# Performance work log

Measured on AMD Instinct MI355X. Metric: run time of the kernel, lower is better.

Reference implementation:

```python
import jax, jax.numpy as jnp
import numpy as np

B, HW, D, CL, K, V, NL, H = 16, 4096, 512, 768, 512, 512, 32, 8
EPS = 1e-5

def conv1d(x, w, b):
    # 1x1 Conv1d: x (B, Cin, L), w (Cout, Cin), b (Cout,)
    return jnp.einsum('oi,bil->bol', w, x) + b[:, None]

def inorm(x):
    # InstanceNorm1d (affine=False, biased var) over the length dim per channel
    m = jnp.mean(x, axis=-1, keepdims=True)
    v = jnp.var(x, axis=-1, keepdims=True)
    return (x - m) / jnp.sqrt(v + EPS)

def _forward(x, l, l_mask, w_vis, b_vis, w_langp, b_langp, w_q, b_q, w_k, b_k,
             w_v, b_v, w_lv, b_lv, w_W, b_W, w_langW, b_langW,
             w_mm, b_mm, w_langmm, b_langmm):
    xt = x.transpose(0, 2, 1)                       # (B, D, HW)
    mask = l_mask.transpose(0, 2, 1)                # (B, 1, NL)
    vis = jax.nn.gelu(conv1d(xt, w_vis, b_vis), approximate=False)      # (B, D, HW)
    lang = jax.nn.gelu(conv1d(l, w_langp, b_langp), approximate=False)  # (B, CL, NL)

    q = inorm(conv1d(xt, w_q, b_q)).transpose(0, 2, 1)   # (B, HW, K)
    k = conv1d(l, w_k, b_k) * mask                       # (B, K, NL)
    v = conv1d(l, w_v, b_v) * mask                       # (B, V, NL)
    lv = inorm(conv1d(xt, w_lv, b_lv))                   # (B, CL, HW)

    q = q.reshape(B, HW, H, K // H).transpose(0, 2, 1, 3)   # (B, H, HW, dk)
    k = k.reshape(B, H, K // H, NL)
    v = v.reshape(B, H, V // H, NL)
    lv = lv.reshape(B, H, CL // H, HW)

    # note: scale uses FULL key_channels (as in the torch code), mask bias added once
    sim = jnp.einsum('bhqd,bhdn->bhqn', q, k) * (K ** -0.5)
    sim = sim + (10000.0 * mask[:, :, None, :] - 10000.0)    # (B, H, HW, NL)

    att = jax.nn.softmax(sim, axis=-1)                         # image -> lang
    latt = jax.nn.softmax(sim.transpose(0, 1, 3, 2), axis=-1)  # lang -> image

    lang_out = jnp.einsum('bhnq,bhcq->bhcn', latt, lv).reshape(B, CL, NL) * mask
    lang_out = inorm(conv1d(lang_out, w_langW, b_langW))       # (B, CL, NL)

    out = jnp.einsum('bhqn,bhdn->bqhd', att, v).reshape(B, HW, V)
    vis_out = inorm(conv1d(out.transpose(0, 2, 1), w_W, b_W))  # (B, V, HW)

    mm = jax.nn.gelu(conv1d(vis * vis_out, w_mm, b_mm), approximate=False)
    lang_mm = jax.nn.gelu(conv1d(lang * lang_out, w_langmm, b_langmm), approximate=False)
    return mm.transpose(0, 2, 1), lang_mm.transpose(0, 2, 1)   # (B,HW,V), (B,NL,CL)

def setup_inputs():
    key = jax.random.key(0)
    ks = jax.random.split(key, 24)
    inp = {}
    inp['x'] = jax.random.normal(ks[0], (B, HW, D), jnp.float32)
    inp['l'] = jax.random.normal(ks[1], (B, CL, NL), jnp.float32)
    lengths = jax.random.randint(ks[2], (B, 1), 5, NL + 1)
    inp['l_mask'] = (jnp.arange(NL)[None, :] < lengths).astype(jnp.float32)[:, :, None]
    specs = [('vis', D, D), ('langp', CL, CL), ('q', K, D), ('k', K, CL),
             ('v', V, CL), ('lv', CL, D), ('W', V, V), ('langW', CL, CL),
             ('mm', V, V), ('langmm', CL, CL)]
    for i, (n, o, ci) in enumerate(specs):
        inp['w_' + n] = jax.random.normal(ks[3 + 2 * i], (o, ci), jnp.float32) / float(np.sqrt(ci))
        inp['b_' + n] = jax.random.normal(ks[4 + 2 * i], (o,), jnp.float32) * 0.01
    return inp

def reference(x, l, l_mask, w_vis, b_vis, w_langp, b_langp, w_q, b_q, w_k, b_k,
              w_v, b_v, w_lv, b_lv, w_W, b_W, w_langW, b_langW,
              w_mm, b_mm, w_langmm, b_langmm):
    return _forward(x, l, l_mask, w_vis, b_vis, w_langp, b_langp, w_q, b_q, w_k, b_k,
                    w_v, b_v, w_lv, b_lv, w_W, b_W, w_langW, b_langW,
                    w_mm, b_mm, w_langmm, b_langmm)
```

## Files before the change

### kernel.cpp

```cpp
#include <hip/hip_runtime.h>
#include <cstdint>
#include <cstddef>


typedef __bf16 bf16x8 __attribute__((ext_vector_type(8)));
typedef float f32x4 __attribute__((ext_vector_type(4)));
typedef unsigned short ushort8 __attribute__((ext_vector_type(8)));
typedef unsigned short us4 __attribute__((ext_vector_type(4)));

__device__ __forceinline__ float bf2f(unsigned short u) {
  union { unsigned int i; float f; } c; c.i = ((unsigned int)u) << 16; return c.f;
}
__device__ __forceinline__ unsigned short f2bf(float f) {
  union { float f; unsigned int i; } c; c.f = f;
  unsigned int r = c.i + 0x7FFFu + ((c.i >> 16) & 1u);
  return (unsigned short)(r >> 16);
}
__device__ __forceinline__ float gelu_f(float x) {
  return 0.5f * x * (1.f + erff(x * 0.70710678118654752f));
}
__device__ __forceinline__ void gload16(const void* g, void* l) {
  __builtin_amdgcn_global_load_lds(
      (__attribute__((address_space(1))) unsigned int*)g,
      (__attribute__((address_space(3))) unsigned int*)l, 16, 0, 0);
}
__device__ __forceinline__ int xcd_swizzle(int orig, int nwg) {
  int qd = nwg >> 3, r = nwg & 7;
  int xcd = orig & 7, idx = orig >> 3;
  return (xcd < r ? xcd * (qd + 1) : r * (qd + 1) + (xcd - r) * qd) + idx;
}

constexpr size_t OFF_SRQ  = 0;
constexpr size_t OFF_SRLV = OFF_SRQ  + (size_t)16*512*2*4;
constexpr size_t OFF_SRW  = OFF_SRLV + (size_t)16*768*2*4;
constexpr size_t OFF_LACC = OFF_SRW  + (size_t)16*512*2*4;
constexpr size_t SZ_ZERO  = OFF_LACC + (size_t)16*768*32*4;
constexpr size_t OFF_KBUF = SZ_ZERO;
constexpr size_t OFF_VBUF = OFF_KBUF + (size_t)16*512*32*4;
constexpr size_t OFF_LANG = OFF_VBUF + (size_t)16*512*32*4;
constexpr size_t OFF_P2   = OFF_LANG + (size_t)16*768*32*4;
constexpr size_t OFF_PMX  = OFF_P2   + (size_t)16*768*32*4;
constexpr size_t OFF_PSM  = OFF_PMX  + (size_t)32*128*32*4;
constexpr size_t OFF_WB   = OFF_PSM  + (size_t)32*128*32*4;
constexpr size_t OFF_Q    = OFF_WB   + (size_t)1441792*2;
constexpr size_t OFF_LV   = OFF_Q    + (size_t)65536*512*2;
constexpr size_t OFF_SIMB = OFF_LV   + (size_t)65536*768*2;

__global__ __launch_bounds__(256) void prep_kernel(
    const float* __restrict__ x,
    const float* __restrict__ w_vis, const float* __restrict__ w_q,
    const float* __restrict__ w_lv, const float* __restrict__ w_W,
    const float* __restrict__ w_mm,
    unsigned short* __restrict__ xb, unsigned short* __restrict__ wb,
    const float* __restrict__ l,
    const float* __restrict__ w_langp, const float* __restrict__ b_langp,
    const float* __restrict__ w_k, const float* __restrict__ b_k,
    const float* __restrict__ w_v, const float* __restrict__ b_v,
    const float* __restrict__ lmask,
    float* __restrict__ lang, float* __restrict__ kbuf, float* __restrict__ vbuf,
    float* __restrict__ zbase)
{
  const int bid = blockIdx.x, t = threadIdx.x;
  if (bid < 17088) {
    int i = bid * 256 + t;
    if (i >= 4374528) return;
    const float* src;
    unsigned short* dst;
    if (i < 4194304) { src = x + (size_t)i * 8; dst = xb + (size_t)i * 8; }
    else {
      int j = i - 4194304;
      dst = wb + (size_t)j * 8;
      if (j < 32768)       src = w_vis + (size_t)j * 8;
      else if (j < 65536)  src = w_q  + (size_t)(j - 32768) * 8;
      else if (j < 114688) src = w_lv + (size_t)(j - 65536) * 8;
      else if (j < 147456) src = w_W  + (size_t)(j - 114688) * 8;
      else                 src = w_mm + (size_t)(j - 147456) * 8;
    }
    const f32x4* s = (const f32x4*)src;
    f32x4 a = s[0], b2 = s[1];
    ushort8 o;
#pragma unroll
    for (int j = 0; j < 4; ++j) { o[j] = f2bf(a[j]); o[j + 4] = f2bf(b2[j]); }
    *(ushort8*)dst = o;
  } else if (bid < 20672) {
    int sb = bid - 17088;
    int b = sb & 15, og = sb >> 4;
    int ol = t >> 5, n = t & 31;
    const float* lb = l + (size_t)b * 768 * 32 + n;
    const float* wr;
    float bv;
    float* out;
    bool gel;
    if (og < 96) {
      int o = og * 8 + ol;
      wr = w_langp + (size_t)o * 768; bv = b_langp[o];
      out = &lang[((size_t)b * 768 + o) * 32 + n]; gel = true;
    } else if (og < 160) {
      int o = (og - 96) * 8 + ol;
      wr = w_k + (size_t)o * 768; bv = b_k[o];
      out = &kbuf[((size_t)b * 512 + o) * 32 + n]; gel = false;
    } else {
      int o = (og - 160) * 8 + ol;
      wr = w_v + (size_t)o * 768; bv = b_v[o];
      out = &vbuf[((size_t)b * 512 + o) * 32 + n]; gel = false;
    }
    float s = 0.f;
#pragma unroll 4
    for (int i = 0; i < 768; ++i) s += wr[i] * lb[(size_t)i * 32];
    s += bv;
    s = gel ? gelu_f(s) : s * lmask[b * 32 + n];
    *out = s;
  } else {
    size_t i = (size_t)(bid - 20672) * 256 + t;
    const f32x4 z = {0.f, 0.f, 0.f, 0.f};
    ((f32x4*)zbase)[i] = z;
  }
}

template<bool GELU, bool STATS, bool OUTF32>
__global__ __launch_bounds__(256) void gemm_bt(
    const unsigned short* __restrict__ A, const unsigned short* __restrict__ Wb,
    const float* __restrict__ bias, void* __restrict__ Yout,
    float* __restrict__ statsraw, int N, int Kd, int nbn)
{
  __shared__ __align__(16) unsigned short As[2][128 * 64];
  __shared__ __align__(16) unsigned short Bs[2][128 * 64];
  const int t = threadIdx.x;
  const int wave = t >> 6, lane = t & 63;
  const int ln = lane & 15, quad = lane >> 4;
  const int wgid = xcd_swizzle(blockIdx.x, gridDim.x);
  const int mt = wgid / nbn, nt = wgid - mt * nbn;
  const int m0 = mt * 128, n0 = nt * 128;
  const int wm = (wave >> 1) * 64, wn = (wave & 1) * 64;
  const f32x4 fzero = {0.f, 0.f, 0.f, 0.f};
  f32x4 acc[4][4];
#pragma unroll
  for (int i = 0; i < 4; ++i)
#pragma unroll
    for (int j = 0; j < 4; ++j) acc[i][j] = fzero;
  const int lrow = lane >> 3;
  const int lch  = lane & 7;
  const unsigned short* Arow = A  + (size_t)(m0 + wave * 32 + lrow) * Kd + lch * 8;
  const unsigned short* Brow = Wb + (size_t)(n0 + wave * 32 + lrow) * Kd + lch * 8;

#define STAGE_BT(buf, k0)                                                     \
  {                                                                           \
    _Pragma("unroll")                                                         \
    for (int it = 0; it < 4; ++it) {                                          \
      int g = wave * 4 + it;                                                  \
      gload16(Arow + (size_t)(it * 8) * Kd + (k0), &As[buf][g * 512]);        \
      gload16(Brow + (size_t)(it * 8) * Kd + (k0), &Bs[buf][g * 512]);        \
    }                                                                         \
  }

  const int NT = Kd >> 6;
  STAGE_BT(0, 0)
  __syncthreads();
  int cur = 0;
  for (int kt = 0; kt < NT; ++kt) {
    if (kt + 1 < NT) STAGE_BT(cur ^ 1, (kt + 1) * 64)
#pragma unroll
    for (int kk = 0; kk < 64; kk += 32) {
      int c = (kk >> 3) + quad;
      bf16x8 af[4], bfr[4];
#pragma unroll
      for (int i = 0; i < 4; ++i)
        af[i] = *(const bf16x8*)&As[cur][(wm + i * 16 + ln) * 64 + c * 8];
#pragma unroll
      for (int j = 0; j < 4; ++j)
        bfr[j] = *(const bf16x8*)&Bs[cur][(wn + j * 16 + ln) * 64 + c * 8];
#pragma unroll
      for (int i = 0; i < 4; ++i)
#pragma unroll
        for (int j = 0; j < 4; ++j)
          acc[i][j] = __builtin_amdgcn_mfma_f32_16x16x32_bf16(af[i], bfr[j], acc[i][j], 0, 0, 0);
    }
    __syncthreads();
    cur ^= 1;
  }
  float bb[4];
#pragma unroll
  for (int j = 0; j < 4; ++j) bb[j] = bias[n0 + wn + j * 16 + ln];
#pragma unroll
  for (int i = 0; i < 4; ++i)
#pragma unroll
    for (int j = 0; j < 4; ++j)
#pragma unroll
      for (int r = 0; r < 4; ++r) {
        float v = acc[i][j][r] + bb[j];
        if (GELU) v = gelu_f(v);
        acc[i][j][r] = v;
        size_t row = (size_t)(m0 + wm + i * 16 + quad * 4 + r);
        size_t idx = row * N + (n0 + wn + j * 16 + ln);
        if (OUTF32) ((float*)Yout)[idx] = v;
        else ((unsigned short*)Yout)[idx] = f2bf(v);
      }
  if (STATS) {
    float* cs = (float*)As;
    cs[t] = 0.f;
    __syncthreads();
#pragma unroll
    for (int j = 0; j < 4; ++j) {
      float s = 0.f, s2 = 0.f;
#pragma unroll
      for (int i = 0; i < 4; ++i)
#pragma unroll
        for (int r = 0; r < 4; ++r) { float v = acc[i][j][r]; s += v; s2 += v * v; }
      s  += __shfl_xor(s, 16);  s  += __shfl_xor(s, 32);
      s2 += __shfl_xor(s2, 16); s2 += __shfl_xor(s2, 32);
      if (quad == 0) {
        int cl = wn + j * 16 + ln;
        atomicAdd(&cs[cl], s);
        atomicAdd(&cs[128 + cl], s2);
      }
    }
    __syncthreads();
    int bIdx = m0 >> 12;
    if (t < 128) atomicAdd(&statsraw[((size_t)bIdx * N + n0 + t) * 2], cs[t]);
    else atomicAdd(&statsraw[((size_t)bIdx * N + n0 + (t - 128)) * 2 + 1], cs[t]);
  }
}

__global__ __launch_bounds__(256) void gemm_fused3(
    const unsigned short* __restrict__ A, const unsigned short* __restrict__ Wcat,
    const float* __restrict__ b_vis, const float* __restrict__ b_q, const float* __restrict__ b_lv,
    unsigned short* __restrict__ visb, unsigned short* __restrict__ qout,
    unsigned short* __restrict__ lvout, float* __restrict__ srq, float* __restrict__ srlv)
{
  constexpr int NBN = 14, Kd = 512;
  __shared__ __align__(16) unsigned short As[2][128 * 64];
  __shared__ __align__(16) unsigned short Bs[2][128 * 64];
  const int t = threadIdx.x;
  const int wave = t >> 6, lane = t & 63;
  const int ln = lane & 15, quad = lane >> 4;
  const int wgid = xcd_swizzle(blockIdx.x, gridDim.x);
  const int mt = wgid / NBN, nt = wgid - mt * NBN;
  const int m0 = mt * 128, n0 = nt * 128;
  const int wm = (wave >> 1) * 64, wn = (wave & 1) * 64;
  const f32x4 fzero = {0.f, 0.f, 0.f, 0.f};
  f32x4 acc[4][4];
#pragma unroll
  for (int i = 0; i < 4; ++i)
#pragma unroll
    for (int j = 0; j < 4; ++j) acc[i][j] = fzero;
  const int lrow = lane >> 3;
  const int lch  = lane & 7;
  const unsigned short* Arow = A    + (size_t)(m0 + wave * 32 + lrow) * Kd + lch * 8;
  const unsigned short* Brow = Wcat + (size_t)(n0 + wave * 32 + lrow) * Kd + lch * 8;

  constexpr int NT = Kd >> 6;
  STAGE_BT(0, 0)
  __syncthreads();
  int cur = 0;
  for (int kt = 0; kt < NT; ++kt) {
    if (kt + 1 < NT) STAGE_BT(cur ^ 1, (kt + 1) * 64)
#pragma unroll
    for (int kk = 0; kk < 64; kk += 32) {
      int c = (kk >> 3) + quad;
      bf16x8 af[4], bfr[4];
#pragma unroll
      for (int i = 0; i < 4; ++i)
        af[i] = *(const bf16x8*)&As[cur][(wm + i * 16 + ln) * 64 + c * 8];
#pragma unroll
      for (int j = 0; j < 4; ++j)
        bfr[j] = *(const bf16x8*)&Bs[cur][(wn + j * 16 + ln) * 64 + c * 8];
#pragma unroll
      for (int i = 0; i < 4; ++i)
#pragma unroll
        for (int j = 0; j < 4; ++j)
          acc[i][j] = __builtin_amdgcn_mfma_f32_16x16x32_bf16(af[i], bfr[j], acc[i][j], 0, 0, 0);
    }
    __syncthreads();
    cur ^= 1;
  }
  int seg = (nt < 4) ? 0 : (nt < 8 ? 1 : 2);
  const float* bias = (seg == 0) ? b_vis : (seg == 1 ? b_q : b_lv);
  unsigned short* Y = (seg == 0) ? visb : (seg == 1 ? qout : lvout);
  float* statsraw   = (seg == 1) ? srq : srlv;
  const int nbase   = n0 - ((seg == 0) ? 0 : (seg == 1 ? 512 : 1024));
  const int Nseg    = (seg == 2) ? 768 : 512;

  float bb[4];
#pragma unroll
  for (int j = 0; j < 4; ++j) bb[j] = bias[nbase + wn + j * 16 + ln];
#pragma unroll
  for (int i = 0; i < 4; ++i)
#pragma unroll
    for (int j = 0; j < 4; ++j)
#pragma unroll
      for (int r = 0; r < 4; ++r) {
        float v = acc[i][j][r] + bb[j];
        if (seg == 0) v = gelu_f(v);
        acc[i][j][r] = v;
        size_t row = (size_t)(m0 + wm + i * 16 + quad * 4 + r);
        Y[row * Nseg + (nbase + wn + j * 16 + ln)] = f2bf(v);
      }
  if (seg != 0) {
    float* cs = (float*)As;
    cs[t] = 0.f;
    __syncthreads();
#pragma unroll
    for (int j = 0; j < 4; ++j) {
      float s = 0.f, s2 = 0.f;
#pragma unroll
      for (int i = 0; i < 4; ++i)
#pragma unroll
        for (int r = 0; r < 4; ++r) { float v = acc[i][j][r]; s += v; s2 += v * v; }
      s  += __shfl_xor(s, 16);  s  += __shfl_xor(s, 32);
      s2 += __shfl_xor(s2, 16); s2 += __shfl_xor(s2, 32);
      if (quad == 0) {
        int cl = wn + j * 16 + ln;
        atomicAdd(&cs[cl], s);
        atomicAdd(&cs[128 + cl], s2);
      }
    }
    __syncthreads();
    int bIdx = m0 >> 12;
    if (t < 128) atomicAdd(&statsraw[((size_t)bIdx * Nseg + nbase + t) * 2], cs[t]);
    else atomicAdd(&statsraw[((size_t)bIdx * Nseg + nbase + (t - 128)) * 2 + 1], cs[t]);
  }
}

__global__ __launch_bounds__(256) void simattv_kernel(
    const unsigned short* __restrict__ qraw, const float* __restrict__ srq,
    const float* __restrict__ kbuf, const float* __restrict__ vbuf,
    const float* __restrict__ lmask,
    unsigned short* __restrict__ simb, unsigned short* __restrict__ outb,
    float* __restrict__ pmx, float* __restrict__ psm)
{
  __shared__ __align__(16) unsigned short kThi[32][72];
  __shared__ __align__(16) unsigned short kTlo[32][72];
  __shared__ __align__(16) unsigned short vshi[64][40];
  __shared__ __align__(16) unsigned short vslo[64][40];
  __shared__ __align__(16) unsigned short pq[4][32][40];
  __shared__ float sm[64], srs[64], cb[32];
  __shared__ float wmax[4][32], wsum[4][32];

  const int qc = blockIdx.x, q0 = qc * 128, h = blockIdx.y, b = blockIdx.z;
  const int bh = b * 8 + h;
  const int t = threadIdx.x;
  const int wv = t >> 6, lane = t & 63, ln = lane & 15, quad = lane >> 4;
  const float scale = 0.04419417382415922f;

  if (t < 64) {
    float s  = srq[(b * 512 + h * 64 + t) * 2];
    float s2 = srq[(b * 512 + h * 64 + t) * 2 + 1];
    float mean = s * (1.f / 4096.f);
    float var  = fmaxf(s2 * (1.f / 4096.f) - mean * mean, 0.f);
    sm[t]  = mean;
    srs[t] = rsqrtf(var + 1e-5f) * scale;
  }
  __syncthreads();

  const float* kb = kbuf + ((size_t)b * 512 + h * 64) * 32;
  const float* vb = vbuf + ((size_t)b * 512 + h * 64) * 32;
  for (int e = t; e < 2048; e += 256) {
    int d = e >> 5, n = e & 31;
    float kv = kb[e] * srs[d];
    unsigned short khi = f2bf(kv);
    kThi[n][d] = khi;
    kTlo[n][d] = f2bf(kv - bf2f(khi));
    float vv = vb[e];
    unsigned short vhi = f2bf(vv);
    vshi[d][n] = vhi;
    vslo[d][n] = f2bf(vv - bf2f(vhi));
  }
  if (t < 32) {
    float s = 0.f;
#pragma unroll 8
    for (int d = 0; d < 64; ++d) s += sm[d] * srs[d] * kb[d * 32 + t];
    cb[t] = 10000.f * (lmask[b * 32 + t] - 1.f) - s;
  }

  const unsigned short* qbase = qraw + ((size_t)(b * 4096) + q0 + wv * 32) * 512 + h * 64;
  bf16x8 qfr[2][2];
#pragma unroll
  for (int qf = 0; qf < 2; ++qf)
#pragma unroll
    for (int kf = 0; kf < 2; ++kf)
      qfr[qf][kf] = *(const bf16x8*)(qbase + (size_t)(qf * 16 + ln) * 512 + kf * 32 + quad * 8);
  __syncthreads();

  const f32x4 fz = {0.f, 0.f, 0.f, 0.f};
  f32x4 accS[2][2] = {{fz, fz}, {fz, fz}};
#pragma unroll
  for (int kf = 0; kf < 2; ++kf) {
#pragma unroll
    for (int nf = 0; nf < 2; ++nf) {
      bf16x8 kh = *(const bf16x8*)&kThi[nf * 16 + ln][kf * 32 + quad * 8];
      bf16x8 kl = *(const bf16x8*)&kTlo[nf * 16 + ln][kf * 32 + quad * 8];
#pragma unroll
      for (int qf = 0; qf < 2; ++qf) {
        accS[qf][nf] = __builtin_amdgcn_mfma_f32_16x16x32_bf16(qfr[qf][kf], kh, accS[qf][nf], 0, 0, 0);
        accS[qf][nf] = __builtin_amdgcn_mfma_f32_16x16x32_bf16(qfr[qf][kf], kl, accS[qf][nf], 0, 0, 0);
      }
    }
  }
  float cb0 = cb[ln], cb1 = cb[16 + ln];
#pragma unroll
  for (int qf = 0; qf < 2; ++qf)
#pragma unroll
    for (int r = 0; r < 4; ++r) {
      accS[qf][0][r] += cb0;
      accS[qf][1][r] += cb1;
    }
  {
    unsigned short* sgb = simb + ((size_t)bh * 4096 + q0 + wv * 32) * 32;
#pragma unroll
    for (int qf = 0; qf < 2; ++qf)
#pragma unroll
      for (int r = 0; r < 4; ++r) {
        size_t rowo = (size_t)(qf * 16 + quad * 4 + r) * 32;
        sgb[rowo + ln]      = f2bf(accS[qf][0][r]);
        sgb[rowo + 16 + ln] = f2bf(accS[qf][1][r]);
      }
  }
#pragma unroll
  for (int nf = 0; nf < 2; ++nf) {
    float m = accS[0][nf][0];
#pragma unroll
    for (int r = 1; r < 4; ++r) m = fmaxf(m, accS[0][nf][r]);
#pragma unroll
    for (int r = 0; r < 4; ++r) m = fmaxf(m, accS[1][nf][r]);
    m = fmaxf(m, __shfl_xor(m, 16));
    m = fmaxf(m, __shfl_xor(m, 32));
    float s = 0.f;
#pragma unroll
    for (int qf = 0; qf < 2; ++qf)
#pragma unroll
      for (int r = 0; r < 4; ++r) s += __expf(accS[qf][nf][r] - m);
    s += __shfl_xor(s, 16);
    s += __shfl_xor(s, 32);
    if (quad == 0) { wmax[wv][nf * 16 + ln] = m; wsum[wv][nf * 16 + ln] = s; }
  }
#pragma unroll
  for (int qf = 0; qf < 2; ++qf) {
#pragma unroll
    for (int r = 0; r < 4; ++r) {
      float a0 = accS[qf][0][r], a1 = accS[qf][1][r];
      float m = fmaxf(a0, a1);
      m = fmaxf(m, __shfl_xor(m, 1));
      m = fmaxf(m, __shfl_xor(m, 2));
      m = fmaxf(m, __shfl_xor(m, 4));
      m = fmaxf(m, __shfl_xor(m, 8));
      float e0 = __expf(a0 - m), e1 = __expf(a1 - m);
      float s = e0 + e1;
      s += __shfl_xor(s, 1);
      s += __shfl_xor(s, 2);
      s += __shfl_xor(s, 4);
      s += __shfl_xor(s, 8);
      float inv = 1.f / s;
      int row = qf * 16 + quad * 4 + r;
      pq[wv][row][ln]      = f2bf(e0 * inv);
      pq[wv][row][16 + ln] = f2bf(e1 * inv);
    }
  }
  __syncthreads();
  bf16x8 vfh[4], vfl[4];
#pragma unroll
  for (int mf = 0; mf < 4; ++mf) {
    vfh[mf] = *(const bf16x8*)&vshi[mf * 16 + ln][quad * 8];
    vfl[mf] = *(const bf16x8*)&vslo[mf * 16 + ln][quad * 8];
  }
#pragma unroll
  for (int nf = 0; nf < 2; ++nf) {
    bf16x8 pb = *(const bf16x8*)&pq[wv][nf * 16 + ln][quad * 8];
    f32x4 accO[4] = {fz, fz, fz, fz};
#pragma unroll
    for (int mf = 0; mf < 4; ++mf) {
      accO[mf] = __builtin_amdgcn_mfma_f32_16x16x32_bf16(vfh[mf], pb, accO[mf], 0, 0, 0);
      accO[mf] = __builtin_amdgcn_mfma_f32_16x16x32_bf16(vfl[mf], pb, accO[mf], 0, 0, 0);
    }
    unsigned short* op = outb + ((size_t)(b * 4096) + q0 + wv * 32 + nf * 16 + ln) * 512 + h * 64;
#pragma unroll
    for (int mf = 0; mf < 4; ++mf) {
      us4 o;
#pragma unroll
      for (int r = 0; r < 4; ++r) o[r] = f2bf(accO[mf][r]);
      *(us4*)(op + mf * 16 + quad * 4) = o;
    }
  }
  __syncthreads();
  if (t < 32) {
    float M = wmax[0][t], S = wsum[0][t];
#pragma unroll
    for (int g = 1; g < 4; ++g) {
      float m2 = wmax[g][t], s2 = wsum[g][t];
      if (m2 > M) { S = S * __expf(M - m2) + s2; M = m2; }
      else S += s2 * __expf(m2 - M);
    }
    pmx[((size_t)qc * 128 + bh) * 32 + t] = M;
    psm[((size_t)qc * 128 + bh) * 32 + t] = S;
  }
}

__global__ __launch_bounds__(256) void langout_acc_kernel(
    const unsigned short* __restrict__ simb, const float* __restrict__ pmx,
    const float* __restrict__ psm, const unsigned short* __restrict__ lvraw,
    const float* __restrict__ srlv, float* __restrict__ lacc)
{
  __shared__ __align__(16) float pt[64][32];
  __shared__ __align__(16) float lvt[64][96];
  __shared__ float cm[96], cr[96], lm[32], li[32];
  int bh = blockIdx.x, b = bh >> 3, h = bh & 7;
  int qs0 = blockIdx.y * 512;
  int t = threadIdx.x;
  if (t < 96) {
    float s  = srlv[(b * 768 + h * 96 + t) * 2];
    float s2 = srlv[(b * 768 + h * 96 + t) * 2 + 1];
    float mean = s * (1.f / 4096.f);
    float var  = fmaxf(s2 * (1.f / 4096.f) - mean * mean, 0.f);
    cm[t] = mean;
    cr[t] = rsqrtf(var + 1e-5f);
  } else if (t >= 128 && t < 160) {
    int n = t - 128;
    float M = -1e30f, S = 0.f;
#pragma unroll 4
    for (int c = 0; c < 32; ++c) {
      float m2 = pmx[((size_t)c * 128 + bh) * 32 + n];
      float s2 = psm[((size_t)c * 128 + bh) * 32 + n];
      if (m2 > M) { S = S * __expf(M - m2) + s2; M = m2; }
      else S += s2 * __expf(m2 - M);
    }
    lm[n] = M;
    li[n] = 1.f / S;
  }
  __syncthreads();
  int n = t & 31, cg = t >> 5;
  float acc[12];
#pragma unroll
  for (int r = 0; r < 12; ++r) acc[r] = 0.f;
  for (int c0 = 0; c0 < 512; c0 += 64) {
    if (c0) __syncthreads();
#pragma unroll
    for (int i = 0; i < 8; ++i) {
      int e = t + 256 * i;
      int ql = e >> 5, nn = e & 31;
      float x = bf2f(simb[((size_t)bh * 4096 + qs0 + c0 + ql) * 32 + nn]);
      pt[ql][nn] = __expf(x - lm[nn]) * li[nn];
    }
#pragma unroll
    for (int i = 0; i < 24; ++i) {
      int e = t + 256 * i;
      int ql = e / 96, cc = e % 96;
      float v = bf2f(lvraw[((size_t)(b * 4096) + qs0 + c0 + ql) * 768 + h * 96 + cc]);
      lvt[ql][cc] = (v - cm[cc]) * cr[cc];
    }
    __syncthreads();
    for (int q = 0; q < 64; ++q) {
      float pv = pt[q][n];
      const f32x4* lp = (const f32x4*)&lvt[q][cg * 12];
      f32x4 a0 = lp[0], a1 = lp[1], a2 = lp[2];
      acc[0] += pv * a0[0]; acc[1] += pv * a0[1]; acc[2]  += pv * a0[2]; acc[3]  += pv * a0[3];
      acc[4] += pv * a1[0]; acc[5] += pv * a1[1]; acc[6]  += pv * a1[2]; acc[7]  += pv * a1[3];
      acc[8] += pv * a2[0]; acc[9] += pv * a2[1]; acc[10] += pv * a2[2]; acc[11] += pv * a2[3];
    }
  }
#pragma unroll
  for (int r = 0; r < 12; ++r)
    atomicAdd(&lacc[((size_t)b * 768 + h * 96 + cg * 12 + r) * 32 + n], acc[r]);
}

__global__ __launch_bounds__(256) void prod_kernel(
    const unsigned short* __restrict__ visb, const unsigned short* __restrict__ wraw,
    const float* __restrict__ srw, unsigned short* __restrict__ P)
{
  size_t idx = ((size_t)blockIdx.x * 256 + threadIdx.x) * 8;
  int b = (int)(idx >> 21);
  int c = (int)(idx & 511);
  ushort8 vv = *(const ushort8*)&visb[idx];
  ushort8 wv = *(const ushort8*)&wraw[idx];
  ushort8 pv;
#pragma unroll
  for (int i = 0; i < 8; ++i) {
    float s  = srw[(b * 512 + c + i) * 2];
    float s2 = srw[(b * 512 + c + i) * 2 + 1];
    float mean = s * (1.f / 4096.f);
    float var  = fmaxf(s2 * (1.f / 4096.f) - mean * mean, 0.f);
    float rs   = rsqrtf(var + 1e-5f);
    pv[i] = f2bf(bf2f(vv[i]) * ((bf2f(wv[i]) - mean) * rs));
  }
  *(ushort8*)&P[idx] = pv;
}

__global__ __launch_bounds__(256) void langW_kernel(
    const float* __restrict__ lacc, const float* __restrict__ w,
    const float* __restrict__ bias, const float* __restrict__ lmask,
    const float* __restrict__ lang, float* __restrict__ p2)
{
  int b = blockIdx.x, og = blockIdx.y;
  int ol = threadIdx.x >> 5, n = threadIdx.x & 31;
  int o = og * 8 + ol;
  const float* ab = lacc + (size_t)b * 768 * 32 + n;
  const float* wr = w + (size_t)o * 768;
  float s = 0.f;
#pragma unroll 4
  for (int i = 0; i < 768; ++i) s += wr[i] * ab[(size_t)i * 32];
  float y = s * lmask[b * 32 + n] + bias[o];
  float m = y;
#pragma unroll
  for (int off = 16; off >= 1; off >>= 1) m += __shfl_xor(m, off);
  m *= (1.f / 32.f);
  float d = y - m;
  float vv = d * d;
#pragma unroll
  for (int off = 16; off >= 1; off >>= 1) vv += __shfl_xor(vv, off);
  vv *= (1.f / 32.f);
  size_t idx = ((size_t)b * 768 + o) * 32 + n;
  p2[idx] = lang[idx] * (d * rsqrtf(vv + 1e-5f));
}

__global__ __launch_bounds__(256) void langmm_kernel(
    const float* __restrict__ p2, const float* __restrict__ w,
    const float* __restrict__ bias, float* __restrict__ out1)
{
  int b = blockIdx.x, og = blockIdx.y;
  int ol = threadIdx.x >> 5, n = threadIdx.x & 31;
  int o = og * 8 + ol;
  const float* pb = p2 + (size_t)b * 768 * 32 + n;
  const float* wr = w + (size_t)o * 768;
  float s = 0.f;
#pragma unroll 4
  for (int i = 0; i < 768; ++i) s += wr[i] * pb[(size_t)i * 32];
  s = gelu_f(s + bias[o]);
  __shared__ float tile[8][32];
  tile[ol][n] = s;
  __syncthreads();
  int nn = threadIdx.x >> 3, cl = threadIdx.x & 7;
  out1[((size_t)b * 32 + nn) * 768 + og * 8 + cl] = tile[cl][nn];
}

extern "C" void kernel_launch(void* const* d_in, const int* in_sizes, int n_in,
                              void* d_out, int out_size, void* d_ws, size_t ws_size,
                              hipStream_t stream)
{
  (void)in_sizes; (void)n_in; (void)out_size; (void)ws_size;
  const float* x       = (const float*)d_in[0];
  const float* l       = (const float*)d_in[1];
  const float* lmask   = (const float*)d_in[2];
  const float* w_vis   = (const float*)d_in[3];
  const float* b_vis   = (const float*)d_in[4];
  const float* w_langp = (const float*)d_in[5];
  const float* b_langp = (const float*)d_in[6];
  const float* w_q     = (const float*)d_in[7];
  const float* b_q     = (const float*)d_in[8];
  const float* w_k     = (const float*)d_in[9];
  const float* b_k     = (const float*)d_in[10];
  const float* w_v     = (const float*)d_in[11];
  const float* b_v     = (const float*)d_in[12];
  const float* w_lv    = (const float*)d_in[13];
  const float* b_lv    = (const float*)d_in[14];
  const float* w_W     = (const float*)d_in[15];
  const float* b_W     = (const float*)d_in[16];
  const float* w_langW = (const float*)d_in[17];
  const float* b_langW = (const float*)d_in[18];
  const float* w_mm    = (const float*)d_in[19];
  const float* b_mm    = (const float*)d_in[20];
  const float* w_langmm= (const float*)d_in[21];
  const float* b_langmm= (const float*)d_in[22];

  char* ws = (char*)d_ws;
  float* srq  = (float*)(ws + OFF_SRQ);
  float* srlv = (float*)(ws + OFF_SRLV);
  float* srw  = (float*)(ws + OFF_SRW);
  float* lacc = (float*)(ws + OFF_LACC);
  float* kbuf = (float*)(ws + OFF_KBUF);
  float* vbuf = (float*)(ws + OFF_VBUF);
  float* lang = (float*)(ws + OFF_LANG);
  float* p2   = (float*)(ws + OFF_P2);
  float* pmx  = (float*)(ws + OFF_PMX);
  float* psm  = (float*)(ws + OFF_PSM);
  unsigned short* wb    = (unsigned short*)(ws + OFF_WB);
  unsigned short* wbW   = wb + 917504;
  unsigned short* wbmm  = wb + 1179648;
  unsigned short* qraw  = (unsigned short*)(ws + OFF_Q);
  unsigned short* lvraw = (unsigned short*)(ws + OFF_LV);
  unsigned short* wraw  = (unsigned short*)(ws + OFF_LV);
  unsigned short* simb  = (unsigned short*)(ws + OFF_SIMB);
  float* out0 = (float*)d_out;
  float* out1 = out0 + (size_t)16 * 4096 * 512;
  unsigned short* visb = (unsigned short*)d_out;
  unsigned short* xb   = (unsigned short*)d_out + 33554432;

  prep_kernel<<<21112, 256, 0, stream>>>(x, w_vis, w_q, w_lv, w_W, w_mm, xb, wb,
                                         l, w_langp, b_langp, w_k, b_k, w_v, b_v,
                                         lmask, lang, kbuf, vbuf, (float*)ws);

  gemm_fused3<<<512 * 14, 256, 0, stream>>>(xb, wb, b_vis, b_q, b_lv,
                                            visb, qraw, lvraw, srq, srlv);

  simattv_kernel<<<dim3(32, 8, 16), 256, 0, stream>>>(qraw, srq, kbuf, vbuf, lmask, simb, qraw, pmx, psm);
  langout_acc_kernel<<<dim3(128, 8), 256, 0, stream>>>(simb, pmx, psm, lvraw, srlv, lacc);

  gemm_bt<false, true,  false><<<512 * 4, 256, 0, stream>>>(qraw, wbW, b_W, wraw, srw, 512, 512, 4);
  prod_kernel<<<16384, 256, 0, stream>>>(visb, wraw, srw, qraw);
  gemm_bt<true,  false, true ><<<512 * 4, 256, 0, stream>>>(qraw, wbmm, b_mm, out0, nullptr, 512, 512, 4);

  langW_kernel<<<dim3(16, 96), 256, 0, stream>>>(lacc, w_langW, b_langW, lmask, lang, p2);
  langmm_kernel<<<dim3(16, 96), 256, 0, stream>>>(p2, w_langmm, b_langmm, out1);
}
```

Measured before the change: 1.216 ms.

## Enlarge GEMM tiles to 256x256 with 8 waves and XOR-swizzled LDS layout

The three bf16 MFMA GEMM kernels move from 128x128 tiles with 4 waves to 256x256 tiles with 8 waves. Each wave now computes 128x64, and grids and n-tile counts are adjusted to match. LDS staging uses an XOR swizzle on the 16-byte chunk index so fragment reads avoid bank conflicts. The goal is more operand reuse per byte loaded and fewer LDS conflicts. In exchange it doubles LDS per block to 128KB, which may cap occupancy at one block per CU, adds register pressure, and produces fewer blocks, so the tail is coarser.

```diff
diff --git a/kernel.cpp b/kernel.cpp
--- a/kernel.cpp
+++ b/kernel.cpp
@@ -117,60 +117,64 @@
   }
 }
 
+#define STG256(buf, k0)                                                            \
+  {                                                                                \
+    _Pragma("unroll")                                                              \
+    for (int r = 0; r < 4; ++r) {                                                  \
+      gload16(Asrc + (size_t)(r * 64) * Kd + (k0), &As[buf][r * 4096 + wave * 512]); \
+      gload16(Bsrc + (size_t)(r * 64) * Kd + (k0), &Bs[buf][r * 4096 + wave * 512]); \
+    }                                                                              \
+  }
+
 template<bool GELU, bool STATS, bool OUTF32>
-__global__ __launch_bounds__(256) void gemm_bt(
+__global__ __launch_bounds__(512, 2) void gemm_bt(
     const unsigned short* __restrict__ A, const unsigned short* __restrict__ Wb,
     const float* __restrict__ bias, void* __restrict__ Yout,
     float* __restrict__ statsraw, int N, int Kd, int nbn)
 {
-  __shared__ __align__(16) unsigned short As[2][128 * 64];
-  __shared__ __align__(16) unsigned short Bs[2][128 * 64];
+  __shared__ __align__(16) unsigned short As[2][256 * 64];
+  __shared__ __align__(16) unsigned short Bs[2][256 * 64];
   const int t = threadIdx.x;
   const int wave = t >> 6, lane = t & 63;
   const int ln = lane & 15, quad = lane >> 4;
   const int wgid = xcd_swizzle(blockIdx.x, gridDim.x);
   const int mt = wgid / nbn, nt = wgid - mt * nbn;
-  const int m0 = mt * 128, n0 = nt * 128;
-  const int wm = (wave >> 1) * 64, wn = (wave & 1) * 64;
+  const int m0 = mt * 256, n0 = nt * 256;
+  const int wm = (wave >> 2) * 128;
+  const int wn = (wave & 3) * 64;
   const f32x4 fzero = {0.f, 0.f, 0.f, 0.f};
-  f32x4 acc[4][4];
-#pragma unroll
-  for (int i = 0; i < 4; ++i)
+  f32x4 acc[8][4];
+#pragma unroll
+  for (int i = 0; i < 8; ++i)
 #pragma unroll
     for (int j = 0; j < 4; ++j) acc[i][j] = fzero;
-  const int lrow = lane >> 3;
-  const int lch  = lane & 7;
-  const unsigned short* Arow = A  + (size_t)(m0 + wave * 32 + lrow) * Kd + lch * 8;
-  const unsigned short* Brow = Wb + (size_t)(n0 + wave * 32 + lrow) * Kd + lch * 8;
-
-#define STAGE_BT(buf, k0)                                                     \
-  {                                                                           \
-    _Pragma("unroll")                                                         \
-    for (int it = 0; it < 4; ++it) {                                          \
-      int g = wave * 4 + it;                                                  \
-      gload16(Arow + (size_t)(it * 8) * Kd + (k0), &As[buf][g * 512]);        \
-      gload16(Brow + (size_t)(it * 8) * Kd + (k0), &Bs[buf][g * 512]);        \
-    }                                                                         \
-  }
+  const int srow8 = wave * 8 + (lane >> 3);
+  const int sch2  = (lane & 7) ^ (srow8 & 7);
+  const unsigned short* Asrc = A  + (size_t)(m0 + srow8) * Kd + sch2 * 8;
+  const unsigned short* Bsrc = Wb + (size_t)(n0 + srow8) * Kd + sch2 * 8;
 
   const int NT = Kd >> 6;
-  STAGE_BT(0, 0)
+  STG256(0, 0)
   __syncthreads();
   int cur = 0;
   for (int kt = 0; kt < NT; ++kt) {
-    if (kt + 1 < NT) STAGE_BT(cur ^ 1, (kt + 1) * 64)
-#pragma unroll
-    for (int kk = 0; kk < 64; kk += 32) {
-      int c = (kk >> 3) + quad;
-      bf16x8 af[4], bfr[4];
-#pragma unroll
-      for (int i = 0; i < 4; ++i)
-        af[i] = *(const bf16x8*)&As[cur][(wm + i * 16 + ln) * 64 + c * 8];
-#pragma unroll
-      for (int j = 0; j < 4; ++j)
-        bfr[j] = *(const bf16x8*)&Bs[cur][(wn + j * 16 + ln) * 64 + c * 8];
-#pragma unroll
-      for (int i = 0; i < 4; ++i)
+    if (kt + 1 < NT) STG256(cur ^ 1, (kt + 1) * 64)
+#pragma unroll
+    for (int kk = 0; kk < 2; ++kk) {
+      const int c = kk * 4 + quad;
+      bf16x8 af[8], bfr[4];
+#pragma unroll
+      for (int i = 0; i < 8; ++i) {
+        int R = wm + i * 16 + ln;
+        af[i] = *(const bf16x8*)&As[cur][R * 64 + ((c ^ (R & 7)) & 7) * 8];
+      }
+#pragma unroll
+      for (int j = 0; j < 4; ++j) {
+        int R = wn + j * 16 + ln;
+        bfr[j] = *(const bf16x8*)&Bs[cur][R * 64 + ((c ^ (R & 7)) & 7) * 8];
+      }
+#pragma unroll
+      for (int i = 0; i < 8; ++i)
 #pragma unroll
         for (int j = 0; j < 4; ++j)
           acc[i][j] = __builtin_amdgcn_mfma_f32_16x16x32_bf16(af[i], bfr[j], acc[i][j], 0, 0, 0);
@@ -182,7 +186,7 @@
 #pragma unroll
   for (int j = 0; j < 4; ++j) bb[j] = bias[n0 + wn + j * 16 + ln];
 #pragma unroll
-  for (int i = 0; i < 4; ++i)
+  for (int i = 0; i < 8; ++i)
 #pragma unroll
     for (int j = 0; j < 4; ++j)
 #pragma unroll
@@ -203,7 +207,7 @@
     for (int j = 0; j < 4; ++j) {
       float s = 0.f, s2 = 0.f;
 #pragma unroll
-      for (int i = 0; i < 4; ++i)
+      for (int i = 0; i < 8; ++i)
 #pragma unroll
         for (int r = 0; r < 4; ++r) { float v = acc[i][j][r]; s += v; s2 += v * v; }
       s  += __shfl_xor(s, 16);  s  += __shfl_xor(s, 32);
@@ -211,61 +215,67 @@
       if (quad == 0) {
         int cl = wn + j * 16 + ln;
         atomicAdd(&cs[cl], s);
-        atomicAdd(&cs[128 + cl], s2);
+        atomicAdd(&cs[256 + cl], s2);
       }
     }
     __syncthreads();
     int bIdx = m0 >> 12;
-    if (t < 128) atomicAdd(&statsraw[((size_t)bIdx * N + n0 + t) * 2], cs[t]);
-    else atomicAdd(&statsraw[((size_t)bIdx * N + n0 + (t - 128)) * 2 + 1], cs[t]);
-  }
-}
-
-__global__ __launch_bounds__(256) void gemm_fused3(
+    int col = t & 255;
+    if (t < 256) atomicAdd(&statsraw[((size_t)bIdx * N + n0 + col) * 2], cs[col]);
+    else atomicAdd(&statsraw[((size_t)bIdx * N + n0 + col) * 2 + 1], cs[256 + col]);
+  }
+}
+
+__global__ __launch_bounds__(512, 2) void gemm_fused3(
     const unsigned short* __restrict__ A, const unsigned short* __restrict__ Wcat,
     const float* __restrict__ b_vis, const float* __restrict__ b_q, const float* __restrict__ b_lv,
     unsigned short* __restrict__ visb, unsigned short* __restrict__ qout,
     unsigned short* __restrict__ lvout, float* __restrict__ srq, float* __restrict__ srlv)
 {
-  constexpr int NBN = 14, Kd = 512;
-  __shared__ __align__(16) unsigned short As[2][128 * 64];
-  __shared__ __align__(16) unsigned short Bs[2][128 * 64];
+  constexpr int NBN = 7, Kd = 512;
+  __shared__ __align__(16) unsigned short As[2][256 * 64];
+  __shared__ __align__(16) unsigned short Bs[2][256 * 64];
   const int t = threadIdx.x;
   const int wave = t >> 6, lane = t & 63;
   const int ln = lane & 15, quad = lane >> 4;
   const int wgid = xcd_swizzle(blockIdx.x, gridDim.x);
   const int mt = wgid / NBN, nt = wgid - mt * NBN;
-  const int m0 = mt * 128, n0 = nt * 128;
-  const int wm = (wave >> 1) * 64, wn = (wave & 1) * 64;
+  const int m0 = mt * 256, n0 = nt * 256;
+  const int wm = (wave >> 2) * 128;
+  const int wn = (wave & 3) * 64;
   const f32x4 fzero = {0.f, 0.f, 0.f, 0.f};
-  f32x4 acc[4][4];
-#pragma unroll
-  for (int i = 0; i < 4; ++i)
+  f32x4 acc[8][4];
+#pragma unroll
+  for (int i = 0; i < 8; ++i)
 #pragma unroll
     for (int j = 0; j < 4; ++j) acc[i][j] = fzero;
-  const int lrow = lane >> 3;
-  const int lch  = lane & 7;
-  const unsigned short* Arow = A    + (size_t)(m0 + wave * 32 + lrow) * Kd + lch * 8;
-  const unsigned short* Brow = Wcat + (size_t)(n0 + wave * 32 + lrow) * Kd + lch * 8;
+  const int srow8 = wave * 8 + (lane >> 3);
+  const int sch2  = (lane & 7) ^ (srow8 & 7);
+  const unsigned short* Asrc = A    + (size_t)(m0 + srow8) * Kd + sch2 * 8;
+  const unsigned short* Bsrc = Wcat + (size_t)(n0 + srow8) * Kd + sch2 * 8;
 
   constexpr int NT = Kd >> 6;
-  STAGE_BT(0, 0)
+  STG256(0, 0)
   __syncthreads();
   int cur = 0;
   for (int kt = 0; kt < NT; ++kt) {
-    if (kt + 1 < NT) STAGE_BT(cur ^ 1, (kt + 1) * 64)
-#pragma unroll
-    for (int kk = 0; kk < 64; kk += 32) {
-      int c = (kk >> 3) + quad;
-      bf16x8 af[4], bfr[4];
-#pragma unroll
-      for (int i = 0; i < 4; ++i)
-        af[i] = *(const bf16x8*)&As[cur][(wm + i * 16 + ln) * 64 + c * 8];
-#pragma unroll
-      for (int j = 0; j < 4; ++j)
-        bfr[j] = *(const bf16x8*)&Bs[cur][(wn + j * 16 + ln) * 64 + c * 8];
-#pragma unroll
-      for (int i = 0; i < 4; ++i)
+    if (kt + 1 < NT) STG256(cur ^ 1, (kt + 1) * 64)
+#pragma unroll
+    for (int kk = 0; kk < 2; ++kk) {
+      const int c = kk * 4 + quad;
+      bf16x8 af[8], bfr[4];
+#pragma unroll
+      for (int i = 0; i < 8; ++i) {
+        int R = wm + i * 16 + ln;
+        af[i] = *(const bf16x8*)&As[cur][R * 64 + ((c ^ (R & 7)) & 7) * 8];
+      }
+#pragma unroll
+      for (int j = 0; j < 4; ++j) {
+        int R = wn + j * 16 + ln;
+        bfr[j] = *(const bf16x8*)&Bs[cur][R * 64 + ((c ^ (R & 7)) & 7) * 8];
+      }
+#pragma unroll
+      for (int i = 0; i < 8; ++i)
 #pragma unroll
         for (int j = 0; j < 4; ++j)
           acc[i][j] = __builtin_amdgcn_mfma_f32_16x16x32_bf16(af[i], bfr[j], acc[i][j], 0, 0, 0);
@@ -273,7 +283,7 @@
     __syncthreads();
     cur ^= 1;
   }
-  int seg = (nt < 4) ? 0 : (nt < 8 ? 1 : 2);
+  const int seg = (nt < 2) ? 0 : (nt < 4 ? 1 : 2);
   const float* bias = (seg == 0) ? b_vis : (seg == 1 ? b_q : b_lv);
   unsigned short* Y = (seg == 0) ? visb : (seg == 1 ? qout : lvout);
   float* statsraw   = (seg == 1) ? srq : srlv;
@@ -284,7 +294,7 @@
 #pragma unroll
   for (int j = 0; j < 4; ++j) bb[j] = bias[nbase + wn + j * 16 + ln];
 #pragma unroll
-  for (int i = 0; i < 4; ++i)
+  for (int i = 0; i < 8; ++i)
 #pragma unroll
     for (int j = 0; j < 4; ++j)
 #pragma unroll
@@ -303,7 +313,7 @@
     for (int j = 0; j < 4; ++j) {
       float s = 0.f, s2 = 0.f;
 #pragma unroll
-      for (int i = 0; i < 4; ++i)
+      for (int i = 0; i < 8; ++i)
 #pragma unroll
         for (int r = 0; r < 4; ++r) { float v = acc[i][j][r]; s += v; s2 += v * v; }
       s  += __shfl_xor(s, 16);  s  += __shfl_xor(s, 32);
@@ -311,13 +321,14 @@
       if (quad == 0) {
         int cl = wn + j * 16 + ln;
         atomicAdd(&cs[cl], s);
-        atomicAdd(&cs[128 + cl], s2);
+        atomicAdd(&cs[256 + cl], s2);
       }
     }
     __syncthreads();
     int bIdx = m0 >> 12;
-    if (t < 128) atomicAdd(&statsraw[((size_t)bIdx * Nseg + nbase + t) * 2], cs[t]);
-    else atomicAdd(&statsraw[((size_t)bIdx * Nseg + nbase + (t - 128)) * 2 + 1], cs[t]);
+    int col = t & 255;
+    if (t < 256) atomicAdd(&statsraw[((size_t)bIdx * Nseg + nbase + col) * 2], cs[col]);
+    else atomicAdd(&statsraw[((size_t)bIdx * Nseg + nbase + col) * 2 + 1], cs[256 + col]);
   }
 }
 
@@ -686,15 +697,15 @@
                                          l, w_langp, b_langp, w_k, b_k, w_v, b_v,
                                          lmask, lang, kbuf, vbuf, (float*)ws);
 
-  gemm_fused3<<<512 * 14, 256, 0, stream>>>(xb, wb, b_vis, b_q, b_lv,
-                                            visb, qraw, lvraw, srq, srlv);
+  gemm_fused3<<<256 * 7, 512, 0, stream>>>(xb, wb, b_vis, b_q, b_lv,
+                                           visb, qraw, lvraw, srq, srlv);
 
   simattv_kernel<<<dim3(32, 8, 16), 256, 0, stream>>>(qraw, srq, kbuf, vbuf, lmask, simb, qraw, pmx, psm);
   langout_acc_kernel<<<dim3(128, 8), 256, 0, stream>>>(simb, pmx, psm, lvraw, srlv, lacc);
 
-  gemm_bt<false, true,  false><<<512 * 4, 256, 0, stream>>>(qraw, wbW, b_W, wraw, srw, 512, 512, 4);
+  gemm_bt<false, true,  false><<<256 * 2, 512, 0, stream>>>(qraw, wbW, b_W, wraw, srw, 512, 512, 2);
   prod_kernel<<<16384, 256, 0, stream>>>(visb, wraw, srw, qraw);
-  gemm_bt<true,  false, true ><<<512 * 4, 256, 0, stream>>>(qraw, wbmm, b_mm, out0, nullptr, 512, 512, 4);
+  gemm_bt<true,  false, true ><<<256 * 2, 512, 0, stream>>>(qraw, wbmm, b_mm, out0, nullptr, 512, 512, 2);
 
   langW_kernel<<<dim3(16, 96), 256, 0, stream>>>(lacc, w_langW, b_langW, lmask, lang, p2);
   langmm_kernel<<<dim3(16, 96), 256, 0, stream>>>(p2, w_langmm, b_langmm, out1);
```

Measured after the change: 1.165 ms. 1.04x faster.
